# Optimization experiments

Hardware: AMD Instinct MI355X
Metric: run time of the kernel (lower is better)

## Reference

```python
import jax, jax.numpy as jnp
import numpy as np

N, C, A = 4096, 1000, 64


def setup_inputs() -> dict:
    key = jax.random.key(0)
    k1, k2, k3, k4, k5 = jax.random.split(key, 5)
    weight_m = jax.random.normal(k1, (C, A), dtype=jnp.float32)
    y = jax.random.normal(k2, (N, C), dtype=jnp.float32)
    features = jax.random.normal(k3, (N, A), dtype=jnp.float32)
    target_x = jax.random.randint(k4, (N,), 0, C)
    ratio = jnp.float32(0.5)
    final_conv = jax.random.normal(k5, (N, A, A), dtype=jnp.float32) * 0.1
    return {
        "weight_m": weight_m,
        "y": y,
        "features": features,
        "target_x": target_x,
        "ratio": ratio,
        "final_conv": final_conv,
        "class_num": C,
    }


def reference(weight_m, y, features, target_x, ratio, final_conv, class_num):
    # weight_m: (C, A); y: (N, C); features: (N, A) (only supplies N, A)
    # target_x: (N,) int labels; final_conv: (N, A, A); ratio: scalar
    Wk = weight_m[target_x]                       # (N, A)  gather of label row
    d = weight_m[None, :, :] - Wk[:, None, :]     # (N, C, A) = NxW_ij - NxW_kj

    # sigma1 = ||w_j||^2 - ||w_{y_n}||^2
    w2 = jnp.sum(weight_m * weight_m, axis=-1)    # (C,)
    sigma1 = w2[None, :] - w2[target_x][:, None]  # (N, C)

    # sigma2 = ratio * diag(d @ CV @ d^T), computed directly (no NxCxC matrix)
    t = jnp.einsum('nca,nab->ncb', d, final_conv)  # (N, C, A)
    sigma2 = ratio * jnp.sum(t * d, axis=-1)       # (N, C)

    logits = y + 0.5 * sigma2 + sigma1             # (N, C)

    # mean cross-entropy (nn.CrossEntropyLoss default)
    logp = jax.nn.log_softmax(logits, axis=-1)
    nll = -jnp.take_along_axis(logp, target_x[:, None], axis=1)[:, 0]
    loss = jnp.mean(nll)
    return loss, y
```

## Files before the change

kernel.cpp:

```cpp
#include <hip/hip_runtime.h>
#include <hip/hip_bf16.h>
#include <stdint.h>
#include <stddef.h>

#define N_    4096
#define C_    1000
#define CP    1024
#define A_    64
#define KPACK 2080
#define KCROSS (KPACK + 64)
#define KTOT  2176
#define KHALF 1088
#define MS    68

typedef __bf16 bf16_2 __attribute__((ext_vector_type(2)));
typedef __bf16 bf16_8 __attribute__((ext_vector_type(8)));
typedef float  f32_4  __attribute__((ext_vector_type(4)));

__device__ __forceinline__ void gl2lds16(const void* g, void* l) {
  __builtin_amdgcn_global_load_lds(
      (const __attribute__((address_space(1))) void*)g,
      (__attribute__((address_space(3))) void*)l, 16, 0, 0);
}

__device__ __forceinline__ void unpack_pair(int k, int& a, int& b) {
  a = (int)(0.5f * (129.0f - sqrtf((float)(16641 - 8 * k))));
  if (a < 0) a = 0;
  while ((a + 1) * (129 - (a + 1)) / 2 <= k) ++a;
  while (a * (129 - a) / 2 > k) --a;
  b = k - a * (129 - a) / 2 + a;
}

__global__ __launch_bounds__(256) void prep_all(
    const float* __restrict__ W, const int* __restrict__ tgt,
    const float* __restrict__ CV, __bf16* __restrict__ Bo,
    float* __restrict__ w2, __bf16* __restrict__ Aq, float* __restrict__ qn) {
  __shared__ float Ms[64 * MS];
  __shared__ float up[4 * 64];
  __shared__ float wk[64];
  __shared__ float us[64];
  int t = threadIdx.x;

  if (blockIdx.x < 1024) {
    int c = blockIdx.x;
    float* ws = Ms;
    if (t < 64) {
      float w = (c < C_) ? W[c * 64 + t] : 0.f;
      ws[t] = w;
      float s = w * w;
      for (int o = 32; o; o >>= 1) s += __shfl_down(s, o);
      if (t == 0 && c < C_) w2[c] = s;
    }
    __syncthreads();
    __bf16* row = Bo + (size_t)c * KTOT;
    for (int p = t; p < KPACK / 2; p += 256) {
      int k = 2 * p;
      int a0, b0, a1, b1;
      unpack_pair(k, a0, b0);
      if (b0 == 63) { a1 = a0 + 1; b1 = a1; } else { a1 = a0; b1 = b0 + 1; }
      bf16_2 v;
      v[0] = (__bf16)(ws[a0] * ws[b0]);
      v[1] = (__bf16)(ws[a1] * ws[b1]);
      *(bf16_2*)(row + k) = v;
    }
    if (t < 64) row[KPACK + t] = (__bf16)ws[t];
    if (t >= 64 && t < 96) row[KCROSS + (t - 64)] = (__bf16)0.f;
  } else {
    int n = blockIdx.x - 1024;
    int lbl = tgt[n];
    if (t < 64) wk[t] = W[lbl * 64 + t];
    const float4* M4 = (const float4*)(CV + (size_t)n * 4096);
    for (int j = 0; j < 4; ++j) {
      int i4 = t + j * 256;
      int r = i4 >> 4, c4 = (i4 & 15) << 2;
      *(float4*)&Ms[r * MS + c4] = M4[i4];
    }
    __syncthreads();
    {
      int a = t & 63, seg = t >> 6;
      float acc = 0.f;
      for (int b = seg * 16; b < seg * 16 + 16; ++b)
        acc += (Ms[a * MS + b] + Ms[b * MS + a]) * wk[b];
      up[seg * 64 + a] = acc;
    }
    __syncthreads();
    if (t < 64) {
      float u = up[t] + up[64 + t] + up[128 + t] + up[192 + t];
      us[t] = u;
      float p = wk[t] * u;
      for (int o = 32; o; o >>= 1) p += __shfl_down(p, o);
      if (t == 0) qn[n] = 0.5f * p;
    }
    __syncthreads();
    __bf16* row = Aq + (size_t)n * KTOT;
    for (int p = t; p < KPACK / 2; p += 256) {
      int k = 2 * p;
      int a0, b0, a1, b1;
      unpack_pair(k, a0, b0);
      if (b0 == 63) { a1 = a0 + 1; b1 = a1; } else { a1 = a0; b1 = b0 + 1; }
      bf16_2 v;
      v[0] = (__bf16)((a0 == b0) ? Ms[a0 * MS + a0]
                                 : (Ms[a0 * MS + b0] + Ms[b0 * MS + a0]));
      v[1] = (__bf16)((a1 == b1) ? Ms[a1 * MS + a1]
                                 : (Ms[a1 * MS + b1] + Ms[b1 * MS + a1]));
      *(bf16_2*)(row + k) = v;
    }
    if (t < 64) row[KPACK + t] = (__bf16)(-us[t]);
    if (t >= 64 && t < 96) row[KCROSS + (t - 64)] = (__bf16)0.f;
  }
}

#define BM 128
#define BN 128
#define BK 64
__global__ __launch_bounds__(256) void gemm_s(const __bf16* __restrict__ Aq,
                                              const __bf16* __restrict__ Bo,
                                              float* __restrict__ Sbase,
                                              int khalf) {
  __shared__ __bf16 As[BM * BK];
  __shared__ __bf16 Bs[BN * BK];
  int t = threadIdx.x;
  int lane = t & 63;
  int w = t >> 6;
  int wr = w & 1;
  int wc = w >> 1;
  int rowBase = blockIdx.y * BM;
  int colBase = blockIdx.x * BN;
  int kb = blockIdx.z * khalf;
  int ke = kb + khalf;
  float* S = Sbase + (size_t)blockIdx.z * ((size_t)N_ * CP);

  f32_4 acc[4][4];
  for (int mi = 0; mi < 4; ++mi)
    for (int ni = 0; ni < 4; ++ni)
      acc[mi][ni] = (f32_4){0.f, 0.f, 0.f, 0.f};

  int m0 = lane & 15;
  int qsw = m0 & 7;

  for (int k0 = kb; k0 < ke; k0 += BK) {
    __syncthreads();
    for (int r = 0; r < 4; ++r) {
      int ch = r * 256 + t;
      int row_p = ch >> 3, qp = ch & 7;
      int q_log = qp ^ (row_p & 7);
      const __bf16* g = Aq + (size_t)(rowBase + row_p) * KTOT + k0 + (q_log << 3);
      gl2lds16(g, As + ch * 8);
    }
    for (int r = 0; r < 4; ++r) {
      int ch = r * 256 + t;
      int row_p = ch >> 3, qp = ch & 7;
      int q_log = qp ^ (row_p & 7);
      const __bf16* g = Bo + (size_t)(colBase + row_p) * KTOT + k0 + (q_log << 3);
      gl2lds16(g, Bs + ch * 8);
    }
    __syncthreads();
    for (int kk = 0; kk < BK; kk += 32) {
      int qbase = (kk >> 3) + (lane >> 4);
      int qphys = qbase ^ qsw;
      bf16_8 af[4], bf[4];
      for (int mi = 0; mi < 4; ++mi)
        af[mi] = *(const bf16_8*)&As[(wr * 64 + mi * 16 + m0) * BK + (qphys << 3)];
      for (int ni = 0; ni < 4; ++ni)
        bf[ni] = *(const bf16_8*)&Bs[(wc * 64 + ni * 16 + m0) * BK + (qphys << 3)];
      for (int mi = 0; mi < 4; ++mi)
        for (int ni = 0; ni < 4; ++ni)
          acc[mi][ni] = __builtin_amdgcn_mfma_f32_16x16x32_bf16(af[mi], bf[ni], acc[mi][ni], 0, 0, 0);
    }
  }

  int ccol = lane & 15;
  int rrow = (lane >> 4) * 4;
  for (int mi = 0; mi < 4; ++mi)
    for (int ni = 0; ni < 4; ++ni) {
      int r0 = rowBase + wr * 64 + mi * 16 + rrow;
      int c0 = colBase + wc * 64 + ni * 16 + ccol;
      for (int j = 0; j < 4; ++j)
        S[(size_t)(r0 + j) * CP + c0] = acc[mi][ni][j];
    }
}

__global__ __launch_bounds__(256) void epilogue(
    const float* __restrict__ S0, const float* __restrict__ S1, int split,
    const float* __restrict__ y, const float* __restrict__ w2,
    const float* __restrict__ qn, const int* __restrict__ tgt,
    const float* __restrict__ ratio_p, float* __restrict__ nll) {
  int t = threadIdx.x, lane = t & 63, w = t >> 6;
  int n = blockIdx.x * 4 + w;
  float hr = 0.5f * (*ratio_p);
  int lbl = tgt[n];
  float q = qn[n];
  float w2k = w2[lbl];
  const float4* S0r = (const float4*)(S0 + (size_t)n * CP);
  const float4* S1r = (const float4*)(S1 + (size_t)n * CP);
  const float4* w24 = (const float4*)w2;
  const float* yr = y + (size_t)n * C_;
  float l[16];
  float mx = -1e30f;
  for (int i = 0; i < 4; ++i) {
    int idx = i * 64 + lane;
    float4 s0 = S0r[idx];
    float4 s1 = split ? S1r[idx] : (float4){0.f, 0.f, 0.f, 0.f};
    float4 w4 = w24[idx];
    int c = idx * 4;
    float sv[4] = {s0.x + s1.x, s0.y + s1.y, s0.z + s1.z, s0.w + s1.w};
    float wv[4] = {w4.x, w4.y, w4.z, w4.w};
    for (int j = 0; j < 4; ++j) {
      float v = -1e30f;
      if (c + j < C_)
        v = yr[c + j] + (wv[j] - w2k) + hr * (sv[j] + q);
      l[i * 4 + j] = v;
      mx = fmaxf(mx, v);
    }
  }
  for (int o = 32; o; o >>= 1) mx = fmaxf(mx, __shfl_xor(mx, o));
  float se = 0.f, lt = 0.f;
  for (int i = 0; i < 4; ++i) {
    int c = (i * 64 + lane) * 4;
    for (int j = 0; j < 4; ++j) {
      float v = l[i * 4 + j];
      se += expf(v - mx);
      lt += (c + j == lbl) ? v : 0.f;
    }
  }
  for (int o = 32; o; o >>= 1) {
    se += __shfl_xor(se, o);
    lt += __shfl_xor(lt, o);
  }
  if (lane == 0) nll[n] = (mx + logf(se)) - lt;
}

__global__ void reduce_loss(const float* __restrict__ nll, float* __restrict__ out) {
  int t = threadIdx.x;
  float s = 0.f;
  for (int i = t; i < N_; i += 256) s += nll[i];
  for (int o = 32; o; o >>= 1) s += __shfl_down(s, o);
  __shared__ float r[4];
  if ((t & 63) == 0) r[t >> 6] = s;
  __syncthreads();
  if (t == 0) out[0] = (r[0] + r[1] + r[2] + r[3]) * (1.0f / (float)N_);
}

extern "C" void kernel_launch(void* const* d_in, const int* in_sizes, int n_in,
                              void* d_out, int out_size, void* d_ws, size_t ws_size,
                              hipStream_t stream) {
  const float* W     = (const float*)d_in[0];
  const float* y     = (const float*)d_in[1];
  const int*   tgt   = (const int*)d_in[3];
  const float* ratio = (const float*)d_in[4];
  const float* CV    = (const float*)d_in[5];

  char* ws = (char*)d_ws;
  size_t off = 0;
  __bf16* Aq = (__bf16*)(ws + off); off += (size_t)N_ * KTOT * sizeof(__bf16);
  __bf16* Bo = (__bf16*)(ws + off); off += (size_t)CP * KTOT * sizeof(__bf16);
  float*  S0 = (float*)(ws + off);  off += (size_t)N_ * CP * sizeof(float);
  size_t off_nosplit = off;
  float*  S1 = (float*)(ws + off);
  size_t off_split = off + (size_t)N_ * CP * sizeof(float);

  size_t tail = 4096 + (size_t)N_ * sizeof(float) * 2;
  int split = (ws_size >= off_split + tail) ? 1 : 0;
  off = split ? off_split : off_nosplit;
  float* w2  = (float*)(ws + off);  off += 4096;
  float* qn  = (float*)(ws + off);  off += (size_t)N_ * sizeof(float);
  float* nll = (float*)(ws + off);  off += (size_t)N_ * sizeof(float);

  float* out = (float*)d_out;
  hipMemcpyAsync(out + 1, y, (size_t)N_ * C_ * sizeof(float),
                 hipMemcpyDeviceToDevice, stream);

  prep_all<<<1024 + N_, 256, 0, stream>>>(W, tgt, CV, Bo, w2, Aq, qn);
  if (split)
    gemm_s<<<dim3(CP / BN, N_ / BM, 2), 256, 0, stream>>>(Aq, Bo, S0, KHALF);
  else
    gemm_s<<<dim3(CP / BN, N_ / BM, 1), 256, 0, stream>>>(Aq, Bo, S0, KTOT);
  epilogue<<<N_ / 4, 256, 0, stream>>>(S0, S1, split, y, w2, qn, tgt, ratio, nll);
  reduce_loss<<<1, 256, 0, stream>>>(nll, out);
}
```

Baseline: 182.0 us.

## Use 4-way split-K GEMM with bf16 partial sums and drop fallback path

The GEMM is now split four ways along K instead of two, with K padded up to a multiple of four BK tiles and the pad zero-filled in prep. Each split writes its partial results as bf16 rather than fp32, so four partial buffers take the same space as two fp32 ones. The epilogue reads and sums the four bf16 partials with 8-wide vector loads. This raises grid parallelism from 512 to 1024 blocks and keeps the partial-sum traffic flat. In exchange it adds rounding error in the partials, adds padded K work, and removes the non-split fallback that was used when the workspace is small.

```diff
diff --git a/kernel.cpp b/kernel.cpp
--- a/kernel.cpp
+++ b/kernel.cpp
@@ -9,8 +9,8 @@
 #define A_    64
 #define KPACK 2080
 #define KCROSS (KPACK + 64)
-#define KTOT  2176
-#define KHALF 1088
+#define KTOT  2304
+#define KQ    576
 #define MS    68
 
 typedef __bf16 bf16_2 __attribute__((ext_vector_type(2)));
@@ -64,7 +64,7 @@
       *(bf16_2*)(row + k) = v;
     }
     if (t < 64) row[KPACK + t] = (__bf16)ws[t];
-    if (t >= 64 && t < 96) row[KCROSS + (t - 64)] = (__bf16)0.f;
+    for (int z2 = t; z2 < KTOT - KCROSS; z2 += 256) row[KCROSS + z2] = (__bf16)0.f;
   } else {
     int n = blockIdx.x - 1024;
     int lbl = tgt[n];
@@ -106,7 +106,7 @@
       *(bf16_2*)(row + k) = v;
     }
     if (t < 64) row[KPACK + t] = (__bf16)(-us[t]);
-    if (t >= 64 && t < 96) row[KCROSS + (t - 64)] = (__bf16)0.f;
+    for (int z2 = t; z2 < KTOT - KCROSS; z2 += 256) row[KCROSS + z2] = (__bf16)0.f;
   }
 }
 
@@ -115,8 +115,7 @@
 #define BK 64
 __global__ __launch_bounds__(256) void gemm_s(const __bf16* __restrict__ Aq,
                                               const __bf16* __restrict__ Bo,
-                                              float* __restrict__ Sbase,
-                                              int khalf) {
+                                              __bf16* __restrict__ Sbase) {
   __shared__ __bf16 As[BM * BK];
   __shared__ __bf16 Bs[BN * BK];
   int t = threadIdx.x;
@@ -126,9 +125,8 @@
   int wc = w >> 1;
   int rowBase = blockIdx.y * BM;
   int colBase = blockIdx.x * BN;
-  int kb = blockIdx.z * khalf;
-  int ke = kb + khalf;
-  float* S = Sbase + (size_t)blockIdx.z * ((size_t)N_ * CP);
+  int kb = blockIdx.z * KQ;
+  __bf16* S = Sbase + (size_t)blockIdx.z * ((size_t)N_ * CP);
 
   f32_4 acc[4][4];
   for (int mi = 0; mi < 4; ++mi)
@@ -138,7 +136,7 @@
   int m0 = lane & 15;
   int qsw = m0 & 7;
 
-  for (int k0 = kb; k0 < ke; k0 += BK) {
+  for (int k0 = kb; k0 < kb + KQ; k0 += BK) {
     __syncthreads();
     for (int r = 0; r < 4; ++r) {
       int ch = r * 256 + t;
@@ -176,51 +174,51 @@
       int r0 = rowBase + wr * 64 + mi * 16 + rrow;
       int c0 = colBase + wc * 64 + ni * 16 + ccol;
       for (int j = 0; j < 4; ++j)
-        S[(size_t)(r0 + j) * CP + c0] = acc[mi][ni][j];
+        S[(size_t)(r0 + j) * CP + c0] = (__bf16)acc[mi][ni][j];
     }
 }
 
 __global__ __launch_bounds__(256) void epilogue(
-    const float* __restrict__ S0, const float* __restrict__ S1, int split,
-    const float* __restrict__ y, const float* __restrict__ w2,
-    const float* __restrict__ qn, const int* __restrict__ tgt,
-    const float* __restrict__ ratio_p, float* __restrict__ nll) {
+    const __bf16* __restrict__ Sb, const float* __restrict__ y,
+    const float* __restrict__ w2, const float* __restrict__ qn,
+    const int* __restrict__ tgt, const float* __restrict__ ratio_p,
+    float* __restrict__ nll) {
   int t = threadIdx.x, lane = t & 63, w = t >> 6;
   int n = blockIdx.x * 4 + w;
   float hr = 0.5f * (*ratio_p);
   int lbl = tgt[n];
   float q = qn[n];
   float w2k = w2[lbl];
-  const float4* S0r = (const float4*)(S0 + (size_t)n * CP);
-  const float4* S1r = (const float4*)(S1 + (size_t)n * CP);
-  const float4* w24 = (const float4*)w2;
+  const bf16_8* S0 = (const bf16_8*)(Sb + (size_t)n * CP);
+  const bf16_8* S1 = (const bf16_8*)(Sb + 1ull * N_ * CP + (size_t)n * CP);
+  const bf16_8* S2 = (const bf16_8*)(Sb + 2ull * N_ * CP + (size_t)n * CP);
+  const bf16_8* S3 = (const bf16_8*)(Sb + 3ull * N_ * CP + (size_t)n * CP);
   const float* yr = y + (size_t)n * C_;
   float l[16];
   float mx = -1e30f;
-  for (int i = 0; i < 4; ++i) {
+  for (int i = 0; i < 2; ++i) {
     int idx = i * 64 + lane;
-    float4 s0 = S0r[idx];
-    float4 s1 = split ? S1r[idx] : (float4){0.f, 0.f, 0.f, 0.f};
-    float4 w4 = w24[idx];
-    int c = idx * 4;
-    float sv[4] = {s0.x + s1.x, s0.y + s1.y, s0.z + s1.z, s0.w + s1.w};
-    float wv[4] = {w4.x, w4.y, w4.z, w4.w};
-    for (int j = 0; j < 4; ++j) {
+    bf16_8 a0 = S0[idx], a1 = S1[idx], a2 = S2[idx], a3 = S3[idx];
+    int c0 = idx * 8;
+    for (int j = 0; j < 8; ++j) {
+      int c = c0 + j;
       float v = -1e30f;
-      if (c + j < C_)
-        v = yr[c + j] + (wv[j] - w2k) + hr * (sv[j] + q);
-      l[i * 4 + j] = v;
+      if (c < C_) {
+        float s = (float)a0[j] + (float)a1[j] + (float)a2[j] + (float)a3[j];
+        v = yr[c] + (w2[c] - w2k) + hr * (s + q);
+      }
+      l[i * 8 + j] = v;
       mx = fmaxf(mx, v);
     }
   }
   for (int o = 32; o; o >>= 1) mx = fmaxf(mx, __shfl_xor(mx, o));
   float se = 0.f, lt = 0.f;
-  for (int i = 0; i < 4; ++i) {
-    int c = (i * 64 + lane) * 4;
-    for (int j = 0; j < 4; ++j) {
-      float v = l[i * 4 + j];
+  for (int i = 0; i < 2; ++i) {
+    int c0 = (i * 64 + lane) * 8;
+    for (int j = 0; j < 8; ++j) {
+      float v = l[i * 8 + j];
       se += expf(v - mx);
-      lt += (c + j == lbl) ? v : 0.f;
+      lt += (c0 + j == lbl) ? v : 0.f;
     }
   }
   for (int o = 32; o; o >>= 1) {
@@ -254,14 +252,7 @@
   size_t off = 0;
   __bf16* Aq = (__bf16*)(ws + off); off += (size_t)N_ * KTOT * sizeof(__bf16);
   __bf16* Bo = (__bf16*)(ws + off); off += (size_t)CP * KTOT * sizeof(__bf16);
-  float*  S0 = (float*)(ws + off);  off += (size_t)N_ * CP * sizeof(float);
-  size_t off_nosplit = off;
-  float*  S1 = (float*)(ws + off);
-  size_t off_split = off + (size_t)N_ * CP * sizeof(float);
-
-  size_t tail = 4096 + (size_t)N_ * sizeof(float) * 2;
-  int split = (ws_size >= off_split + tail) ? 1 : 0;
-  off = split ? off_split : off_nosplit;
+  __bf16* S  = (__bf16*)(ws + off); off += 4ull * N_ * CP * sizeof(__bf16);
   float* w2  = (float*)(ws + off);  off += 4096;
   float* qn  = (float*)(ws + off);  off += (size_t)N_ * sizeof(float);
   float* nll = (float*)(ws + off);  off += (size_t)N_ * sizeof(float);
@@ -271,10 +262,7 @@
                  hipMemcpyDeviceToDevice, stream);
 
   prep_all<<<1024 + N_, 256, 0, stream>>>(W, tgt, CV, Bo, w2, Aq, qn);
-  if (split)
-    gemm_s<<<dim3(CP / BN, N_ / BM, 2), 256, 0, stream>>>(Aq, Bo, S0, KHALF);
-  else
-    gemm_s<<<dim3(CP / BN, N_ / BM, 1), 256, 0, stream>>>(Aq, Bo, S0, KTOT);
-  epilogue<<<N_ / 4, 256, 0, stream>>>(S0, S1, split, y, w2, qn, tgt, ratio, nll);
+  gemm_s<<<dim3(CP / BN, N_ / BM, 4), 256, 0, stream>>>(Aq, Bo, S);
+  epilogue<<<N_ / 4, 256, 0, stream>>>(S, y, w2, qn, tgt, ratio, nll);
   reduce_loss<<<1, 256, 0, stream>>>(nll, out);
 }
```

Result: slower. 188.8 us (+3.7%).
